# Kernel tuning notes

Measured on AMD Instinct MI355X. Metric: run time of the kernel, lower is better.

The kernel has to match this reference:

```python
import jax, jax.numpy as jnp
import numpy as np

RESET_ALPHA = 0.9
THR_ALPHA = 0.95
DAMPENING = 0.3
REFRACTORY = 5


def setup_inputs() -> dict:
    key = jax.random.key(0)
    B, T, N = 16, 4096, 1024
    x = jax.random.normal(key, (B, T, N), dtype=jnp.float32)
    return {
        "x": x,
        "reset_gamma": jnp.ones((N,), jnp.float32),
        "thr_gamma": jnp.ones((N,), jnp.float32),
        "u0": jnp.zeros((N,), jnp.float32),
        "b0": jnp.zeros((N,), jnp.float32),
    }


def _spike(v):
    # SpikeFunction: heaviside forward, piecewise-quadratic surrogate gradient
    zf = (v > 0).astype(v.dtype)
    zb = jnp.where(v > 0, -0.5 * jnp.square(v - 1.0), 0.5 * jnp.square(v + 1.0))
    zb = jnp.where(jnp.abs(v) < 1.0, zb, 0.0) * DAMPENING
    # value == zf, gradient flows through zb (straight-through surrogate)
    return jax.lax.stop_gradient(zf - zb) + zb


def reference(x, reset_gamma, thr_gamma, u0, b0):
    B, T, N = x.shape
    al, bet = RESET_ALPHA, THR_ALPHA

    def step(carry, xt):
        u, b, q, last_z = carry  # all [B, N]
        u = al * u + (1.0 - al) * xt - last_z * reset_gamma
        z = _spike(u - b)
        z = jnp.where(q == 0, z, jnp.zeros_like(z))  # refractory mask
        q = jnp.maximum(0, q - 1)
        q = q + REFRACTORY * jax.lax.stop_gradient(z).astype(jnp.int32)
        b = bet * b + (1.0 - bet) * z * thr_gamma
        return (u, b, q, z), z

    u = jnp.broadcast_to(u0[None, :], (B, N)).astype(x.dtype)
    b = jnp.broadcast_to(b0[None, :], (B, N)).astype(x.dtype)
    q = jnp.zeros((B, N), jnp.int32)
    last_z = jnp.zeros((B, N), x.dtype)

    x_tbn = jnp.swapaxes(x, 0, 1)  # [T, B, N] for scan over time
    _, zs = jax.lax.scan(step, (u, b, q, last_z), x_tbn)
    return jnp.swapaxes(zs, 0, 1)  # [B, T, N]
```

## Files before the change

### kernel.cpp

```cpp
#include <hip/hip_runtime.h>


#pragma STDC FP_CONTRACT OFF

constexpr int B_LEN = 16;
constexpr int T_LEN = 4096;
constexpr int N_LEN = 1024;
constexpr int U     = 32;
constexpr int NCH   = T_LEN / U;

#define FPB(x) asm volatile("" : "+v"(x))

__device__ __forceinline__ void load_chunk(float (&buf)[U],
                                           const float* __restrict__ xp,
                                           int cidx)
{
    const float* p = xp + (size_t)cidx * U * N_LEN;
    #pragma unroll
    for (int i = 0; i < U; ++i) buf[i] = p[(size_t)i * N_LEN];
}

__device__ __forceinline__ void proc_chunk(const float (&buf)[U],
                                           float* __restrict__ p,
                                           float rg, float tg,
                                           float& u, float& bb, int& q, float& lz)
{
    #pragma clang fp contract(off)
    #pragma unroll
    for (int i = 0; i < U; ++i) {
        float m2 = 0.1f * buf[i];
        FPB(m2);
        float s1 = __builtin_fmaf(0.9f, u, m2);
        u = __builtin_fmaf(-lz, rg, s1);

        const float v   = u - bb;
        const bool  pos = v > 0.0f;
        const float zf  = pos ? 1.0f : 0.0f;
        const float vm  = pos ? (v - 1.0f) : (v + 1.0f);
        const float sq  = vm * vm;
        float zb = pos ? (-0.5f * sq) : (0.5f * sq);
        zb = (fabsf(v) < 1.0f) ? zb : 0.0f;
        zb = zb * 0.3f;
        FPB(zb);
        float d1 = zf - zb;
        FPB(d1);
        float z = d1 + zb;

        z = (q == 0) ? z : 0.0f;
        q = (q > 0 ? q - 1 : 0) + 5 * (int)z;

        float t1 = 0.05f * z;
        FPB(t1);
        float t2 = t1 * tg;
        FPB(t2);
        bb = __builtin_fmaf(0.95f, bb, t2);

        lz = z;
        p[(size_t)i * N_LEN] = z;
    }
}

__global__ __launch_bounds__(64)
void snn_fwd(const float* __restrict__ x,
             const float* __restrict__ rg_,
             const float* __restrict__ tg_,
             const float* __restrict__ u0_,
             const float* __restrict__ b0_,
             float* __restrict__ out)
{
    const int id = blockIdx.x * blockDim.x + threadIdx.x;
    const int b  = id >> 10;
    const int n  = id & 1023;

    const float rg = rg_[n];
    const float tg = tg_[n];
    float u  = u0_[n];
    float bb = b0_[n];
    int   q  = 0;
    float lz = 0.0f;

    const size_t base = (size_t)b * T_LEN * N_LEN + n;
    const float* xp = x + base;
    float*       op = out + base;

    float bufA[U], bufB[U];

    load_chunk(bufA, xp, 0);

    for (int c = 0; c < NCH; c += 2) {
        load_chunk(bufB, xp, c + 1);
        proc_chunk(bufA, op + (size_t)c * U * N_LEN, rg, tg, u, bb, q, lz);

        const int c2 = (c + 2 < NCH) ? (c + 2) : (NCH - 1);
        load_chunk(bufA, xp, c2);
        proc_chunk(bufB, op + (size_t)(c + 1) * U * N_LEN, rg, tg, u, bb, q, lz);
    }
}

extern "C" void kernel_launch(void* const* d_in, const int* in_sizes, int n_in,
                              void* d_out, int out_size, void* d_ws, size_t ws_size,
                              hipStream_t stream)
{
    int xi = 0;
    for (int i = 1; i < n_in; ++i)
        if (in_sizes[i] > in_sizes[xi]) xi = i;

    const float* small[4];
    int k = 0;
    for (int i = 0; i < n_in && k < 4; ++i)
        if (i != xi) small[k++] = (const float*)d_in[i];

    const float* x  = (const float*)d_in[xi];
    float*      out = (float*)d_out;

    dim3 block(64);
    dim3 grid(B_LEN * N_LEN / 64);
    snn_fwd<<<grid, block, 0, stream>>>(x, small[0], small[1],
                                        small[2], small[3], out);
}
```

Baseline: 281.4 us.

## Use rolling per-slot prefetch ring and replace refractory counter with allow-time

Replaces the double-buffered chunk load/process with a single rolling register ring, where each slot is refilled with the element DEPTH steps ahead right after it is consumed. This keeps loads in flight continuously instead of in bursts. The refractory countdown is replaced by a next-allowed timestep comparison, which removes the per-step decrement and max. The asm barriers that pinned rounding order are dropped, leaving only fp-contract off, so bit-exactness of the surrogate arithmetic now depends on the compiler.

```diff
diff --git a/kernel.cpp b/kernel.cpp
--- a/kernel.cpp
+++ b/kernel.cpp
@@ -6,59 +6,8 @@
 constexpr int B_LEN = 16;
 constexpr int T_LEN = 4096;
 constexpr int N_LEN = 1024;
-constexpr int U     = 32;
-constexpr int NCH   = T_LEN / U;
-
-#define FPB(x) asm volatile("" : "+v"(x))
-
-__device__ __forceinline__ void load_chunk(float (&buf)[U],
-                                           const float* __restrict__ xp,
-                                           int cidx)
-{
-    const float* p = xp + (size_t)cidx * U * N_LEN;
-    #pragma unroll
-    for (int i = 0; i < U; ++i) buf[i] = p[(size_t)i * N_LEN];
-}
-
-__device__ __forceinline__ void proc_chunk(const float (&buf)[U],
-                                           float* __restrict__ p,
-                                           float rg, float tg,
-                                           float& u, float& bb, int& q, float& lz)
-{
-    #pragma clang fp contract(off)
-    #pragma unroll
-    for (int i = 0; i < U; ++i) {
-        float m2 = 0.1f * buf[i];
-        FPB(m2);
-        float s1 = __builtin_fmaf(0.9f, u, m2);
-        u = __builtin_fmaf(-lz, rg, s1);
-
-        const float v   = u - bb;
-        const bool  pos = v > 0.0f;
-        const float zf  = pos ? 1.0f : 0.0f;
-        const float vm  = pos ? (v - 1.0f) : (v + 1.0f);
-        const float sq  = vm * vm;
-        float zb = pos ? (-0.5f * sq) : (0.5f * sq);
-        zb = (fabsf(v) < 1.0f) ? zb : 0.0f;
-        zb = zb * 0.3f;
-        FPB(zb);
-        float d1 = zf - zb;
-        FPB(d1);
-        float z = d1 + zb;
-
-        z = (q == 0) ? z : 0.0f;
-        q = (q > 0 ? q - 1 : 0) + 5 * (int)z;
-
-        float t1 = 0.05f * z;
-        FPB(t1);
-        float t2 = t1 * tg;
-        FPB(t2);
-        bb = __builtin_fmaf(0.95f, bb, t2);
-
-        lz = z;
-        p[(size_t)i * N_LEN] = z;
-    }
-}
+constexpr int DEPTH = 32;
+constexpr int NCH   = T_LEN / DEPTH;
 
 __global__ __launch_bounds__(64)
 void snn_fwd(const float* __restrict__ x,
@@ -68,32 +17,59 @@
              const float* __restrict__ b0_,
              float* __restrict__ out)
 {
-    const int id = blockIdx.x * blockDim.x + threadIdx.x;
-    const int b  = id >> 10;
-    const int n  = id & 1023;
+    #pragma clang fp contract(off)
+    const int id   = blockIdx.x * blockDim.x + threadIdx.x;
+    const int b    = id >> 10;
+    const int n    = id & 1023;
+    const int loff = b * (T_LEN * N_LEN) + n;
 
     const float rg = rg_[n];
     const float tg = tg_[n];
     float u  = u0_[n];
     float bb = b0_[n];
-    int   q  = 0;
     float lz = 0.0f;
+    int allow = 0;
 
-    const size_t base = (size_t)b * T_LEN * N_LEN + n;
-    const float* xp = x + base;
-    float*       op = out + base;
+    float buf[DEPTH];
+    #pragma unroll
+    for (int i = 0; i < DEPTH; ++i)
+        buf[i] = x[(size_t)i * N_LEN + loff];
 
-    float bufA[U], bufB[U];
+    for (int c = 0; c < NCH; ++c) {
+        #pragma unroll
+        for (int i = 0; i < DEPTH; ++i) {
+            const int   tt = c * DEPTH + i;
+            const float xt = buf[i];
 
-    load_chunk(bufA, xp, 0);
+            int tp = tt + DEPTH;
+            if (tp > T_LEN - 1) tp = T_LEN - 1;
+            buf[i] = x[(size_t)tp * N_LEN + loff];
 
-    for (int c = 0; c < NCH; c += 2) {
-        load_chunk(bufB, xp, c + 1);
-        proc_chunk(bufA, op + (size_t)c * U * N_LEN, rg, tg, u, bb, q, lz);
+            float m2 = 0.1f * xt;
+            float s1 = __builtin_fmaf(0.9f, u, m2);
+            u = __builtin_fmaf(-lz, rg, s1);
 
-        const int c2 = (c + 2 < NCH) ? (c + 2) : (NCH - 1);
-        load_chunk(bufA, xp, c2);
-        proc_chunk(bufB, op + (size_t)(c + 1) * U * N_LEN, rg, tg, u, bb, q, lz);
+            const float v   = u - bb;
+            const bool  pos = v > 0.0f;
+            const float vm = v + (pos ? -1.0f : 1.0f);
+            const float sq = vm * vm;
+            float zb = (pos ? -0.5f : 0.5f) * sq;
+            zb = (fabsf(v) < 1.0f) ? zb : 0.0f;
+            zb = zb * 0.3f;
+            const float zf = pos ? 1.0f : 0.0f;
+            const float d1 = zf - zb;
+            float z = d1 + zb;
+
+            z = (tt >= allow) ? z : 0.0f;
+            allow = (z == 1.0f) ? (tt + 6) : allow;
+
+            float t1 = 0.05f * z;
+            float t2 = t1 * tg;
+            bb = __builtin_fmaf(0.95f, bb, t2);
+
+            lz = z;
+            out[(size_t)tt * N_LEN + loff] = z;
+        }
     }
 }
 
```

After: 404.0 us. 1.44x slower.
